# Optimization experiments

Measured on AMD Instinct MI355X. Metric: run time of the kernel, lower is better.

Reference implementation:

```python
import jax, jax.numpy as jnp
import numpy as np

VOCAB = 1024
ENC_D = 256
PRED_D = 256
JOINT_D = ENC_D + PRED_D


def setup_inputs() -> dict:
    key = jax.random.key(0)
    k1, k2, k3, k4, k5, k6 = jax.random.split(key, 6)
    B, T, U = 8, 256, 64
    encoder_outputs = jax.random.normal(k1, (B, T, ENC_D), dtype=jnp.float32)
    decoder_outputs = jax.random.normal(k2, (B, U, PRED_D), dtype=jnp.float32)
    s1 = 1.0 / np.sqrt(JOINT_D)
    W1 = jax.random.uniform(k3, (JOINT_D, JOINT_D), dtype=jnp.float32, minval=-s1, maxval=s1)
    b1 = jax.random.uniform(k4, (JOINT_D,), dtype=jnp.float32, minval=-s1, maxval=s1)
    W2 = jax.random.uniform(k5, (VOCAB, JOINT_D), dtype=jnp.float32, minval=-s1, maxval=s1)
    b2 = jax.random.uniform(k6, (VOCAB,), dtype=jnp.float32, minval=-s1, maxval=s1)
    return {"encoder_outputs": encoder_outputs, "decoder_outputs": decoder_outputs,
            "W1": W1, "b1": b1, "W2": W2, "b2": b2}


def reference(encoder_outputs, decoder_outputs, W1, b1, W2, b2):
    # Decompose the first linear over the concat: split W1 into enc/dec blocks,
    # project each sequence separately, then broadcast-add over (t, u).
    # This is the same math as cat([enc_rep, dec_rep], -1) @ W1.T + b1.
    W1e = W1[:, :ENC_D]   # [J, E]
    W1d = W1[:, ENC_D:]   # [J, P]
    enc_proj = jnp.einsum('bte,je->btj', encoder_outputs, W1e)  # [B,T,J]
    dec_proj = jnp.einsum('bup,jp->buj', decoder_outputs, W1d)  # [B,U,J]
    h = enc_proj[:, :, None, :] + dec_proj[:, None, :, :] + b1  # [B,T,U,J]
    h = jnp.tanh(h)
    logits = jnp.einsum('btuj,vj->btuv', h, W2) + b2             # [B,T,U,V]
    return jax.nn.log_softmax(logits, axis=-1)
```

## Files before the change

### kernel.cpp

```cpp
#include <hip/hip_runtime.h>
#include <hip/hip_bf16.h>
#include <cstdint>
#include <cstddef>

#define NB 8
#define NT 256
#define NU 64
#define DJ 512
#define DV 1024
#define DK 256

typedef __attribute__((ext_vector_type(8))) short short8;
typedef __attribute__((ext_vector_type(4))) float floatx4;

__device__ __forceinline__ unsigned short f2bf(float x) {
    unsigned int u = __float_as_uint(x);
    u += 0x7fffu + ((u >> 16) & 1u);
    return (unsigned short)(u >> 16);
}

__global__ __launch_bounds__(256) void stage1_gemm(
    const float* __restrict__ enc, const float* __restrict__ dec,
    const float* __restrict__ W1, const float* __restrict__ b1,
    float* __restrict__ enc_proj, float* __restrict__ dec_proj)
{
    __shared__ float As[64][17];
    __shared__ float Bs[16][65];

    const int n0 = blockIdx.x * 64;
    const int m0 = blockIdx.y * 64;
    const bool is_enc = (m0 < NB * NT);
    const float* A = is_enc ? enc : dec;
    const int arow0 = is_enc ? m0 : (m0 - NB * NT);
    const int koff  = is_enc ? 0 : DK;
    float* C = is_enc ? enc_proj : dec_proj;

    const int tid = threadIdx.x;
    const int kk = tid & 15;
    const int grp = tid >> 4;
    const int tx = tid & 15;
    const int ty = tid >> 4;

    float acc[4][4] = {};

    for (int k0 = 0; k0 < DK; k0 += 16) {
        #pragma unroll
        for (int g = 0; g < 4; g++) {
            As[grp + g * 16][kk] = A[(size_t)(arow0 + grp + g * 16) * DK + k0 + kk];
            Bs[kk][grp + g * 16] = W1[(size_t)(n0 + grp + g * 16) * DJ + koff + k0 + kk];
        }
        __syncthreads();
        #pragma unroll
        for (int k = 0; k < 16; k++) {
            float av[4], bv[4];
            #pragma unroll
            for (int i = 0; i < 4; i++) av[i] = As[ty * 4 + i][k];
            #pragma unroll
            for (int j = 0; j < 4; j++) bv[j] = Bs[k][tx * 4 + j];
            #pragma unroll
            for (int i = 0; i < 4; i++)
                #pragma unroll
                for (int j = 0; j < 4; j++)
                    acc[i][j] = fmaf(av[i], bv[j], acc[i][j]);
        }
        __syncthreads();
    }

    float4 bias = make_float4(0.f, 0.f, 0.f, 0.f);
    if (is_enc) bias = *(const float4*)&b1[n0 + tx * 4];
    #pragma unroll
    for (int i = 0; i < 4; i++) {
        const int row = arow0 + ty * 4 + i;
        float4 v;
        v.x = acc[i][0] + bias.x;
        v.y = acc[i][1] + bias.y;
        v.z = acc[i][2] + bias.z;
        v.w = acc[i][3] + bias.w;
        *(float4*)&C[(size_t)row * DJ + n0 + tx * 4] = v;
    }
}

__global__ __launch_bounds__(256) void convert_w2(
    const float* __restrict__ W2, unsigned short* __restrict__ W2b)
{
    const int i = (blockIdx.x * 256 + threadIdx.x) * 4;
    float4 v = *(const float4*)(W2 + i);
    ushort4 o;
    o.x = f2bf(v.x); o.y = f2bf(v.y); o.z = f2bf(v.z); o.w = f2bf(v.w);
    *(ushort4*)(W2b + i) = o;
}

__global__ __launch_bounds__(512, 2) void joint_kernel(
    const float* __restrict__ enc_proj, const float* __restrict__ dec_proj,
    const unsigned short* __restrict__ W2b, const float* __restrict__ b2,
    float* __restrict__ out)
{
    __shared__ __align__(16) unsigned char smem[65536];
    unsigned short* ha = (unsigned short*)smem;

    const int bt = blockIdx.x;
    const int b = bt >> 8;
    const int tid = threadIdx.x;

    {
        const int j0 = (tid & 127) * 4;
        const int ug = tid >> 7;
        const float4 e = *(const float4*)(enc_proj + (size_t)bt * DJ + j0);
        const float* dp = dec_proj + (size_t)(b * NU + ug * 16) * DJ + j0;
        const int chunk = j0 >> 3;
        const int wi = j0 & 7;
        #pragma unroll 4
        for (int i = 0; i < 16; i++) {
            const int u = ug * 16 + i;
            float4 d = *(const float4*)(dp + (size_t)i * DJ);
            float x0 = e.x + d.x, x1 = e.y + d.y, x2 = e.z + d.z, x3 = e.w + d.w;
            ushort4 o;
            o.x = f2bf(1.f - 2.f / (__expf(2.f * x0) + 1.f));
            o.y = f2bf(1.f - 2.f / (__expf(2.f * x1) + 1.f));
            o.z = f2bf(1.f - 2.f / (__expf(2.f * x2) + 1.f));
            o.w = f2bf(1.f - 2.f / (__expf(2.f * x3) + 1.f));
            *(ushort4*)(ha + (size_t)u * DJ + (((chunk ^ (u & 7)) << 3) + wi)) = o;
        }
    }
    __syncthreads();

    const int w = tid >> 6;
    const int lane = tid & 63;
    const int q = lane >> 4;
    const int nn = lane & 15;
    const int wbase = w * 128;

    floatx4 acc[4][8];
    #pragma unroll
    for (int rt = 0; rt < 4; rt++)
        #pragma unroll
        for (int ct = 0; ct < 8; ct++)
            acc[rt][ct] = (floatx4){0.f, 0.f, 0.f, 0.f};

    const unsigned short* pB0 = W2b + (size_t)(wbase + nn * 4) * DJ + q * 8;
    const unsigned short* pB1 = pB0 + (size_t)64 * DJ;

    short8 bv0[8], bv1[8];
    short8 av[4];

    #pragma unroll
    for (int c4 = 0; c4 < 4; c4++) {
        bv0[c4]     = *(const short8*)(pB0 + (size_t)c4 * DJ);
        bv0[4 + c4] = *(const short8*)(pB1 + (size_t)c4 * DJ);
    }

    for (int ks = 0; ks < 16; ks += 2) {
        #pragma unroll
        for (int c4 = 0; c4 < 4; c4++) {
            bv1[c4]     = *(const short8*)(pB0 + (size_t)c4 * DJ + (ks + 1) * 32);
            bv1[4 + c4] = *(const short8*)(pB1 + (size_t)c4 * DJ + (ks + 1) * 32);
        }
        #pragma unroll
        for (int rt = 0; rt < 4; rt++) {
            const int u = rt * 16 + nn;
            const int c = ((ks * 4 + q) ^ (u & 7)) << 3;
            av[rt] = *(const short8*)(ha + (size_t)u * DJ + c);
        }
        #pragma unroll
        for (int ct = 0; ct < 8; ct++)
            #pragma unroll
            for (int rt = 0; rt < 4; rt++)
                acc[rt][ct] = __builtin_amdgcn_mfma_f32_16x16x32_bf16(
                    av[rt], bv0[ct], acc[rt][ct], 0, 0, 0);

        if (ks + 2 < 16) {
            #pragma unroll
            for (int c4 = 0; c4 < 4; c4++) {
                bv0[c4]     = *(const short8*)(pB0 + (size_t)c4 * DJ + (ks + 2) * 32);
                bv0[4 + c4] = *(const short8*)(pB1 + (size_t)c4 * DJ + (ks + 2) * 32);
            }
        }
        #pragma unroll
        for (int rt = 0; rt < 4; rt++) {
            const int u = rt * 16 + nn;
            const int c = (((ks + 1) * 4 + q) ^ (u & 7)) << 3;
            av[rt] = *(const short8*)(ha + (size_t)u * DJ + c);
        }
        #pragma unroll
        for (int ct = 0; ct < 8; ct++)
            #pragma unroll
            for (int rt = 0; rt < 4; rt++)
                acc[rt][ct] = __builtin_amdgcn_mfma_f32_16x16x32_bf16(
                    av[rt], bv1[ct], acc[rt][ct], 0, 0, 0);
    }

    __syncthreads();

    float* wred     = (float*)smem;
    float* rowoff_s = (float*)(smem + 2048);

    float b2a[8];
    *(float4*)&b2a[0] = *(const float4*)(b2 + wbase + nn * 4);
    *(float4*)&b2a[4] = *(const float4*)(b2 + wbase + 64 + nn * 4);
    #pragma unroll
    for (int rt = 0; rt < 4; rt++)
        #pragma unroll
        for (int ct = 0; ct < 8; ct++)
            #pragma unroll
            for (int r = 0; r < 4; r++)
                acc[rt][ct][r] += b2a[ct];

    #pragma unroll
    for (int rt = 0; rt < 4; rt++) {
        #pragma unroll
        for (int r = 0; r < 4; r++) {
            float s = 0.f;
            #pragma unroll
            for (int ct = 0; ct < 8; ct++) s += __expf(acc[rt][ct][r]);
            #pragma unroll
            for (int mk = 1; mk <= 8; mk <<= 1) s += __shfl_xor(s, mk, 64);
            if (nn == 0) wred[(rt * 16 + q * 4 + r) * 8 + w] = s;
        }
    }
    __syncthreads();
    if (tid < 64) {
        float4 s0 = *(const float4*)&wred[tid * 8];
        float4 s1 = *(const float4*)&wred[tid * 8 + 4];
        float s = ((s0.x + s0.y) + (s0.z + s0.w)) + ((s1.x + s1.y) + (s1.z + s1.w));
        rowoff_s[tid] = __logf(s);
    }
    __syncthreads();

    float* outb = out + (size_t)bt * NU * DV;
    #pragma unroll
    for (int rt = 0; rt < 4; rt++) {
        #pragma unroll
        for (int r = 0; r < 4; r++) {
            const int u = rt * 16 + q * 4 + r;
            const float off = rowoff_s[u];
            floatx4 v0, v1;
            v0[0] = acc[rt][0][r] - off; v0[1] = acc[rt][1][r] - off;
            v0[2] = acc[rt][2][r] - off; v0[3] = acc[rt][3][r] - off;
            v1[0] = acc[rt][4][r] - off; v1[1] = acc[rt][5][r] - off;
            v1[2] = acc[rt][6][r] - off; v1[3] = acc[rt][7][r] - off;
            __builtin_nontemporal_store(v0, (floatx4*)(outb + (size_t)u * DV + wbase + nn * 4));
            __builtin_nontemporal_store(v1, (floatx4*)(outb + (size_t)u * DV + wbase + 64 + nn * 4));
        }
    }
}

extern "C" void kernel_launch(void* const* d_in, const int* in_sizes, int n_in,
                              void* d_out, int out_size, void* d_ws, size_t ws_size,
                              hipStream_t stream) {
    const float* enc = (const float*)d_in[0];
    const float* dec = (const float*)d_in[1];
    const float* W1  = (const float*)d_in[2];
    const float* b1  = (const float*)d_in[3];
    const float* W2  = (const float*)d_in[4];
    const float* b2  = (const float*)d_in[5];
    float* out = (float*)d_out;

    float* enc_proj = (float*)d_ws;
    float* dec_proj = enc_proj + (size_t)(NB * NT) * DJ;
    unsigned short* W2b = (unsigned short*)(dec_proj + (size_t)DJ * DJ);

    dim3 g1(8, 40);
    stage1_gemm<<<g1, 256, 0, stream>>>(enc, dec, W1, b1, enc_proj, dec_proj);
    convert_w2<<<512, 256, 0, stream>>>(W2, W2b);
    joint_kernel<<<NB * NT, 512, 0, stream>>>(enc_proj, dec_proj, W2b, b2, out);
}
```

Before: 836.4 us.

## Process four timesteps per block with double-buffered tanh prefetch overlapping MFMA

Each joint-kernel block now iterates over four (b,t) rows and keeps two LDS buffers for the tanh hidden tile. While MFMAs consume the current tile, each thread computes and stores the next row's tanh activations into the other buffer. This is meant to hide the tanh/exp prologue and reduce per-block startup. The LDS footprint more than doubles to ~130KB, which limits residency to one block per CU, and the grid shrinks fourfold, reducing parallelism and latency hiding for the output stores.

```diff
diff --git a/kernel.cpp b/kernel.cpp
--- a/kernel.cpp
+++ b/kernel.cpp
@@ -10,6 +10,8 @@
 #define DV 1024
 #define DK 256
 
+#define TPB 4
+
 typedef __attribute__((ext_vector_type(8))) short short8;
 typedef __attribute__((ext_vector_type(4))) float floatx4;
 
@@ -17,6 +19,16 @@
     unsigned int u = __float_as_uint(x);
     u += 0x7fffu + ((u >> 16) & 1u);
     return (unsigned short)(u >> 16);
+}
+
+__device__ __forceinline__ ushort4 tanh4_bf(float4 e, float4 d) {
+    float x0 = e.x + d.x, x1 = e.y + d.y, x2 = e.z + d.z, x3 = e.w + d.w;
+    ushort4 o;
+    o.x = f2bf(1.f - 2.f / (__expf(2.f * x0) + 1.f));
+    o.y = f2bf(1.f - 2.f / (__expf(2.f * x1) + 1.f));
+    o.z = f2bf(1.f - 2.f / (__expf(2.f * x2) + 1.f));
+    o.w = f2bf(1.f - 2.f / (__expf(2.f * x3) + 1.f));
+    return o;
 }
 
 __global__ __launch_bounds__(256) void stage1_gemm(
@@ -95,151 +107,176 @@
     const unsigned short* __restrict__ W2b, const float* __restrict__ b2,
     float* __restrict__ out)
 {
-    __shared__ __align__(16) unsigned char smem[65536];
+    __shared__ __align__(16) unsigned char smem[133376];
     unsigned short* ha = (unsigned short*)smem;
-
-    const int bt = blockIdx.x;
-    const int b = bt >> 8;
+    float* wred     = (float*)(smem + 131072);
+    float* rowoff_s = (float*)(smem + 133120);
+
+    const int bt0 = blockIdx.x * TPB;
     const int tid = threadIdx.x;
 
-    {
-        const int j0 = (tid & 127) * 4;
-        const int ug = tid >> 7;
-        const float4 e = *(const float4*)(enc_proj + (size_t)bt * DJ + j0);
-        const float* dp = dec_proj + (size_t)(b * NU + ug * 16) * DJ + j0;
-        const int chunk = j0 >> 3;
-        const int wi = j0 & 7;
-        #pragma unroll 4
-        for (int i = 0; i < 16; i++) {
-            const int u = ug * 16 + i;
-            float4 d = *(const float4*)(dp + (size_t)i * DJ);
-            float x0 = e.x + d.x, x1 = e.y + d.y, x2 = e.z + d.z, x3 = e.w + d.w;
-            ushort4 o;
-            o.x = f2bf(1.f - 2.f / (__expf(2.f * x0) + 1.f));
-            o.y = f2bf(1.f - 2.f / (__expf(2.f * x1) + 1.f));
-            o.z = f2bf(1.f - 2.f / (__expf(2.f * x2) + 1.f));
-            o.w = f2bf(1.f - 2.f / (__expf(2.f * x3) + 1.f));
-            *(ushort4*)(ha + (size_t)u * DJ + (((chunk ^ (u & 7)) << 3) + wi)) = o;
-        }
-    }
-    __syncthreads();
+    const int j0 = (tid & 127) * 4;
+    const int ug = tid >> 7;
+    const int chunk = j0 >> 3;
+    const int wi = j0 & 7;
 
     const int w = tid >> 6;
     const int lane = tid & 63;
     const int q = lane >> 4;
     const int nn = lane & 15;
     const int wbase = w * 128;
-
-    floatx4 acc[4][8];
-    #pragma unroll
-    for (int rt = 0; rt < 4; rt++)
-        #pragma unroll
-        for (int ct = 0; ct < 8; ct++)
-            acc[rt][ct] = (floatx4){0.f, 0.f, 0.f, 0.f};
-
     const unsigned short* pB0 = W2b + (size_t)(wbase + nn * 4) * DJ + q * 8;
     const unsigned short* pB1 = pB0 + (size_t)64 * DJ;
 
-    short8 bv0[8], bv1[8];
-    short8 av[4];
-
-    #pragma unroll
-    for (int c4 = 0; c4 < 4; c4++) {
-        bv0[c4]     = *(const short8*)(pB0 + (size_t)c4 * DJ);
-        bv0[4 + c4] = *(const short8*)(pB1 + (size_t)c4 * DJ);
-    }
-
-    for (int ks = 0; ks < 16; ks += 2) {
-        #pragma unroll
-        for (int c4 = 0; c4 < 4; c4++) {
-            bv1[c4]     = *(const short8*)(pB0 + (size_t)c4 * DJ + (ks + 1) * 32);
-            bv1[4 + c4] = *(const short8*)(pB1 + (size_t)c4 * DJ + (ks + 1) * 32);
-        }
-        #pragma unroll
-        for (int rt = 0; rt < 4; rt++) {
-            const int u = rt * 16 + nn;
-            const int c = ((ks * 4 + q) ^ (u & 7)) << 3;
-            av[rt] = *(const short8*)(ha + (size_t)u * DJ + c);
-        }
-        #pragma unroll
-        for (int ct = 0; ct < 8; ct++)
-            #pragma unroll
-            for (int rt = 0; rt < 4; rt++)
-                acc[rt][ct] = __builtin_amdgcn_mfma_f32_16x16x32_bf16(
-                    av[rt], bv0[ct], acc[rt][ct], 0, 0, 0);
-
-        if (ks + 2 < 16) {
-            #pragma unroll
-            for (int c4 = 0; c4 < 4; c4++) {
-                bv0[c4]     = *(const short8*)(pB0 + (size_t)c4 * DJ + (ks + 2) * 32);
-                bv0[4 + c4] = *(const short8*)(pB1 + (size_t)c4 * DJ + (ks + 2) * 32);
-            }
-        }
-        #pragma unroll
-        for (int rt = 0; rt < 4; rt++) {
-            const int u = rt * 16 + nn;
-            const int c = (((ks + 1) * 4 + q) ^ (u & 7)) << 3;
-            av[rt] = *(const short8*)(ha + (size_t)u * DJ + c);
-        }
-        #pragma unroll
-        for (int ct = 0; ct < 8; ct++)
-            #pragma unroll
-            for (int rt = 0; rt < 4; rt++)
-                acc[rt][ct] = __builtin_amdgcn_mfma_f32_16x16x32_bf16(
-                    av[rt], bv1[ct], acc[rt][ct], 0, 0, 0);
-    }
-
-    __syncthreads();
-
-    float* wred     = (float*)smem;
-    float* rowoff_s = (float*)(smem + 2048);
-
-    float b2a[8];
-    *(float4*)&b2a[0] = *(const float4*)(b2 + wbase + nn * 4);
-    *(float4*)&b2a[4] = *(const float4*)(b2 + wbase + 64 + nn * 4);
-    #pragma unroll
-    for (int rt = 0; rt < 4; rt++)
-        #pragma unroll
-        for (int ct = 0; ct < 8; ct++)
-            #pragma unroll
-            for (int r = 0; r < 4; r++)
-                acc[rt][ct][r] += b2a[ct];
-
-    #pragma unroll
-    for (int rt = 0; rt < 4; rt++) {
-        #pragma unroll
-        for (int r = 0; r < 4; r++) {
-            float s = 0.f;
-            #pragma unroll
-            for (int ct = 0; ct < 8; ct++) s += __expf(acc[rt][ct][r]);
-            #pragma unroll
-            for (int mk = 1; mk <= 8; mk <<= 1) s += __shfl_xor(s, mk, 64);
-            if (nn == 0) wred[(rt * 16 + q * 4 + r) * 8 + w] = s;
+    {
+        const int bt = bt0;
+        const int b = bt >> 8;
+        const float4 e = *(const float4*)(enc_proj + (size_t)bt * DJ + j0);
+        const float* dpp = dec_proj + (size_t)(b * NU + ug * 16) * DJ + j0;
+        #pragma unroll 4
+        for (int i2 = 0; i2 < 16; i2++) {
+            const int u = ug * 16 + i2;
+            float4 d = *(const float4*)(dpp + (size_t)i2 * DJ);
+            *(ushort4*)(ha + (size_t)u * DJ + (((chunk ^ (u & 7)) << 3) + wi)) =
+                tanh4_bf(e, d);
         }
     }
     __syncthreads();
-    if (tid < 64) {
-        float4 s0 = *(const float4*)&wred[tid * 8];
-        float4 s1 = *(const float4*)&wred[tid * 8 + 4];
-        float s = ((s0.x + s0.y) + (s0.z + s0.w)) + ((s1.x + s1.y) + (s1.z + s1.w));
-        rowoff_s[tid] = __logf(s);
-    }
-    __syncthreads();
-
-    float* outb = out + (size_t)bt * NU * DV;
-    #pragma unroll
-    for (int rt = 0; rt < 4; rt++) {
-        #pragma unroll
-        for (int r = 0; r < 4; r++) {
-            const int u = rt * 16 + q * 4 + r;
-            const float off = rowoff_s[u];
-            floatx4 v0, v1;
-            v0[0] = acc[rt][0][r] - off; v0[1] = acc[rt][1][r] - off;
-            v0[2] = acc[rt][2][r] - off; v0[3] = acc[rt][3][r] - off;
-            v1[0] = acc[rt][4][r] - off; v1[1] = acc[rt][5][r] - off;
-            v1[2] = acc[rt][6][r] - off; v1[3] = acc[rt][7][r] - off;
-            __builtin_nontemporal_store(v0, (floatx4*)(outb + (size_t)u * DV + wbase + nn * 4));
-            __builtin_nontemporal_store(v1, (floatx4*)(outb + (size_t)u * DV + wbase + 64 + nn * 4));
+
+    for (int t = 0; t < TPB; t++) {
+        const int bt = bt0 + t;
+        const int cur = t & 1;
+        unsigned short* hac = ha + cur * 32768;
+        unsigned short* han = ha + (cur ^ 1) * 32768;
+        const bool hasNext = (t + 1 < TPB);
+
+        float4 e_n = make_float4(0.f, 0.f, 0.f, 0.f);
+        const float* dpn = nullptr;
+        float4 dcur = make_float4(0.f, 0.f, 0.f, 0.f);
+        float4 dnxt;
+        if (hasNext) {
+            const int btn = bt + 1;
+            const int bn = btn >> 8;
+            e_n = *(const float4*)(enc_proj + (size_t)btn * DJ + j0);
+            dpn = dec_proj + (size_t)(bn * NU + ug * 16) * DJ + j0;
+            dcur = *(const float4*)(dpn);
+        }
+
+        floatx4 acc[4][8];
+        #pragma unroll
+        for (int rt = 0; rt < 4; rt++)
+            #pragma unroll
+            for (int ct = 0; ct < 8; ct++)
+                acc[rt][ct] = (floatx4){0.f, 0.f, 0.f, 0.f};
+
+        short8 bv0[8], bv1[8];
+        short8 av[4];
+
+        #pragma unroll
+        for (int c4 = 0; c4 < 4; c4++) {
+            bv0[c4]     = *(const short8*)(pB0 + (size_t)c4 * DJ);
+            bv0[4 + c4] = *(const short8*)(pB1 + (size_t)c4 * DJ);
+        }
+
+        for (int ks = 0; ks < 16; ks += 2) {
+            #pragma unroll
+            for (int c4 = 0; c4 < 4; c4++) {
+                bv1[c4]     = *(const short8*)(pB0 + (size_t)c4 * DJ + (ks + 1) * 32);
+                bv1[4 + c4] = *(const short8*)(pB1 + (size_t)c4 * DJ + (ks + 1) * 32);
+            }
+            if (hasNext) {
+                dnxt = *(const float4*)(dpn + (size_t)(ks + 1) * DJ);
+                const int u = ug * 16 + ks;
+                *(ushort4*)(han + (size_t)u * DJ + (((chunk ^ (u & 7)) << 3) + wi)) =
+                    tanh4_bf(e_n, dcur);
+            }
+            #pragma unroll
+            for (int rt = 0; rt < 4; rt++) {
+                const int u2 = rt * 16 + nn;
+                const int c = ((ks * 4 + q) ^ (u2 & 7)) << 3;
+                av[rt] = *(const short8*)(hac + (size_t)u2 * DJ + c);
+            }
+            #pragma unroll
+            for (int ct = 0; ct < 8; ct++)
+                #pragma unroll
+                for (int rt = 0; rt < 4; rt++)
+                    acc[rt][ct] = __builtin_amdgcn_mfma_f32_16x16x32_bf16(
+                        av[rt], bv0[ct], acc[rt][ct], 0, 0, 0);
+
+            if (ks + 2 < 16) {
+                #pragma unroll
+                for (int c4 = 0; c4 < 4; c4++) {
+                    bv0[c4]     = *(const short8*)(pB0 + (size_t)c4 * DJ + (ks + 2) * 32);
+                    bv0[4 + c4] = *(const short8*)(pB1 + (size_t)c4 * DJ + (ks + 2) * 32);
+                }
+            }
+            if (hasNext) {
+                if (ks + 2 < 16) dcur = *(const float4*)(dpn + (size_t)(ks + 2) * DJ);
+                const int u = ug * 16 + ks + 1;
+                *(ushort4*)(han + (size_t)u * DJ + (((chunk ^ (u & 7)) << 3) + wi)) =
+                    tanh4_bf(e_n, dnxt);
+            }
+            #pragma unroll
+            for (int rt = 0; rt < 4; rt++) {
+                const int u2 = rt * 16 + nn;
+                const int c = (((ks + 1) * 4 + q) ^ (u2 & 7)) << 3;
+                av[rt] = *(const short8*)(hac + (size_t)u2 * DJ + c);
+            }
+            #pragma unroll
+            for (int ct = 0; ct < 8; ct++)
+                #pragma unroll
+                for (int rt = 0; rt < 4; rt++)
+                    acc[rt][ct] = __builtin_amdgcn_mfma_f32_16x16x32_bf16(
+                        av[rt], bv1[ct], acc[rt][ct], 0, 0, 0);
+        }
+
+        float b2a[8];
+        *(float4*)&b2a[0] = *(const float4*)(b2 + wbase + nn * 4);
+        *(float4*)&b2a[4] = *(const float4*)(b2 + wbase + 64 + nn * 4);
+        #pragma unroll
+        for (int rt = 0; rt < 4; rt++)
+            #pragma unroll
+            for (int ct = 0; ct < 8; ct++)
+                #pragma unroll
+                for (int r = 0; r < 4; r++)
+                    acc[rt][ct][r] += b2a[ct];
+
+        #pragma unroll
+        for (int rt = 0; rt < 4; rt++) {
+            #pragma unroll
+            for (int r = 0; r < 4; r++) {
+                float s = 0.f;
+                #pragma unroll
+                for (int ct = 0; ct < 8; ct++) s += __expf(acc[rt][ct][r]);
+                #pragma unroll
+                for (int mk = 1; mk <= 8; mk <<= 1) s += __shfl_xor(s, mk, 64);
+                if (nn == 0) wred[(rt * 16 + q * 4 + r) * 8 + w] = s;
+            }
+        }
+        __syncthreads();
+        if (tid < 64) {
+            float4 s0 = *(const float4*)&wred[tid * 8];
+            float4 s1 = *(const float4*)&wred[tid * 8 + 4];
+            float s = ((s0.x + s0.y) + (s0.z + s0.w)) + ((s1.x + s1.y) + (s1.z + s1.w));
+            rowoff_s[tid] = __logf(s);
+        }
+        __syncthreads();
+
+        float* outb = out + (size_t)bt * NU * DV;
+        #pragma unroll
+        for (int rt = 0; rt < 4; rt++) {
+            #pragma unroll
+            for (int r = 0; r < 4; r++) {
+                const int u = rt * 16 + q * 4 + r;
+                const float off = rowoff_s[u];
+                floatx4 v0, v1;
+                v0[0] = acc[rt][0][r] - off; v0[1] = acc[rt][1][r] - off;
+                v0[2] = acc[rt][2][r] - off; v0[3] = acc[rt][3][r] - off;
+                v1[0] = acc[rt][4][r] - off; v1[1] = acc[rt][5][r] - off;
+                v1[2] = acc[rt][6][r] - off; v1[3] = acc[rt][7][r] - off;
+                __builtin_nontemporal_store(v0, (floatx4*)(outb + (size_t)u * DV + wbase + nn * 4));
+                __builtin_nontemporal_store(v1, (floatx4*)(outb + (size_t)u * DV + wbase + 64 + nn * 4));
+            }
         }
     }
 }
@@ -262,5 +299,5 @@
     dim3 g1(8, 40);
     stage1_gemm<<<g1, 256, 0, stream>>>(enc, dec, W1, b1, enc_proj, dec_proj);
     convert_w2<<<512, 256, 0, stream>>>(W2, W2b);
-    joint_kernel<<<NB * NT, 512, 0, stream>>>(enc_proj, dec_proj, W2b, b2, out);
-}
+    joint_kernel<<<(NB * NT) / TPB, 512, 0, stream>>>(enc_proj, dec_proj, W2b, b2, out);
+}
```

New measurement: 843.5 us. Within noise of the previous version (+0.9%).

## Stage W2 tiles through LDS with async global_load_lds double buffering

Applied to the files above, without the earlier changes.

In the joint kernel, the W2 B-operand is no longer loaded straight from global memory into registers. It is now streamed into per-wave LDS buffers with global_load_lds and read back from LDS before each MFMA block. Two buffers split the columns into a low half and a high half, and explicit vmcnt waits plus sched barriers overlap the next load with the current MFMAs. This reduces register use for B fragments from sixteen to four short8 vectors. In exchange, shared memory per block doubles to 128KB, which likely caps occupancy at one 512-thread block per CU and shortens how far ahead B is prefetched.

```diff
diff --git a/kernel.cpp b/kernel.cpp
--- a/kernel.cpp
+++ b/kernel.cpp
@@ -17,6 +17,12 @@
     unsigned int u = __float_as_uint(x);
     u += 0x7fffu + ((u >> 16) & 1u);
     return (unsigned short)(u >> 16);
+}
+
+__device__ __forceinline__ void gll16(const void* g, void* l) {
+    __builtin_amdgcn_global_load_lds(
+        (const __attribute__((address_space(1))) unsigned int*)g,
+        (__attribute__((address_space(3))) unsigned int*)l, 16, 0, 0);
 }
 
 __global__ __launch_bounds__(256) void stage1_gemm(
@@ -95,8 +101,10 @@
     const unsigned short* __restrict__ W2b, const float* __restrict__ b2,
     float* __restrict__ out)
 {
-    __shared__ __align__(16) unsigned char smem[65536];
+    __shared__ __align__(16) unsigned char smem[131072];
     unsigned short* ha = (unsigned short*)smem;
+    unsigned short* Bb0 = (unsigned short*)(smem + 65536);
+    unsigned short* Bb1 = (unsigned short*)(smem + 98304);
 
     const int bt = blockIdx.x;
     const int b = bt >> 8;
@@ -130,6 +138,13 @@
     const int nn = lane & 15;
     const int wbase = w * 128;
 
+    const unsigned short* gpL = W2b + (size_t)(wbase + nn * 4) * DJ + q * 8;
+    const unsigned short* gpH = gpL + (size_t)64 * DJ;
+
+    unsigned short* ldsL = Bb0 + w * 2048;
+    unsigned short* ldsH = Bb1 + w * 2048;
+    const int lrd = lane * 8;
+
     floatx4 acc[4][8];
     #pragma unroll
     for (int rt = 0; rt < 4; rt++)
@@ -137,56 +152,55 @@
         for (int ct = 0; ct < 8; ct++)
             acc[rt][ct] = (floatx4){0.f, 0.f, 0.f, 0.f};
 
-    const unsigned short* pB0 = W2b + (size_t)(wbase + nn * 4) * DJ + q * 8;
-    const unsigned short* pB1 = pB0 + (size_t)64 * DJ;
-
-    short8 bv0[8], bv1[8];
     short8 av[4];
-
-    #pragma unroll
-    for (int c4 = 0; c4 < 4; c4++) {
-        bv0[c4]     = *(const short8*)(pB0 + (size_t)c4 * DJ);
-        bv0[4 + c4] = *(const short8*)(pB1 + (size_t)c4 * DJ);
-    }
-
-    for (int ks = 0; ks < 16; ks += 2) {
-        #pragma unroll
-        for (int c4 = 0; c4 < 4; c4++) {
-            bv1[c4]     = *(const short8*)(pB0 + (size_t)c4 * DJ + (ks + 1) * 32);
-            bv1[4 + c4] = *(const short8*)(pB1 + (size_t)c4 * DJ + (ks + 1) * 32);
-        }
+    short8 bv[4];
+
+    #pragma unroll
+    for (int c4 = 0; c4 < 4; c4++)
+        gll16(gpL + (size_t)c4 * DJ, ldsL + c4 * 512);
+
+    for (int ks = 0; ks < 16; ks++) {
+        #pragma unroll
+        for (int c4 = 0; c4 < 4; c4++)
+            gll16(gpH + (size_t)c4 * DJ + ks * 32, ldsH + c4 * 512);
+
         #pragma unroll
         for (int rt = 0; rt < 4; rt++) {
-            const int u = rt * 16 + nn;
-            const int c = ((ks * 4 + q) ^ (u & 7)) << 3;
-            av[rt] = *(const short8*)(ha + (size_t)u * DJ + c);
-        }
-        #pragma unroll
-        for (int ct = 0; ct < 8; ct++)
+            const int u2 = rt * 16 + nn;
+            const int c = ((ks * 4 + q) ^ (u2 & 7)) << 3;
+            av[rt] = *(const short8*)(ha + (size_t)u2 * DJ + c);
+        }
+
+        asm volatile("s_waitcnt vmcnt(4)" ::: "memory");
+        __builtin_amdgcn_sched_barrier(0);
+        #pragma unroll
+        for (int c4 = 0; c4 < 4; c4++)
+            bv[c4] = *(const short8*)(ldsL + c4 * 512 + lrd);
+        #pragma unroll
+        for (int c4 = 0; c4 < 4; c4++)
             #pragma unroll
             for (int rt = 0; rt < 4; rt++)
-                acc[rt][ct] = __builtin_amdgcn_mfma_f32_16x16x32_bf16(
-                    av[rt], bv0[ct], acc[rt][ct], 0, 0, 0);
-
-        if (ks + 2 < 16) {
-            #pragma unroll
-            for (int c4 = 0; c4 < 4; c4++) {
-                bv0[c4]     = *(const short8*)(pB0 + (size_t)c4 * DJ + (ks + 2) * 32);
-                bv0[4 + c4] = *(const short8*)(pB1 + (size_t)c4 * DJ + (ks + 2) * 32);
-            }
-        }
-        #pragma unroll
-        for (int rt = 0; rt < 4; rt++) {
-            const int u = rt * 16 + nn;
-            const int c = (((ks + 1) * 4 + q) ^ (u & 7)) << 3;
-            av[rt] = *(const short8*)(ha + (size_t)u * DJ + c);
-        }
-        #pragma unroll
-        for (int ct = 0; ct < 8; ct++)
+                acc[rt][c4] = __builtin_amdgcn_mfma_f32_16x16x32_bf16(
+                    av[rt], bv[c4], acc[rt][c4], 0, 0, 0);
+
+        if (ks + 1 < 16) {
+            #pragma unroll
+            for (int c4 = 0; c4 < 4; c4++)
+                gll16(gpL + (size_t)c4 * DJ + (ks + 1) * 32, ldsL + c4 * 512);
+            asm volatile("s_waitcnt vmcnt(4)" ::: "memory");
+        } else {
+            asm volatile("s_waitcnt vmcnt(0)" ::: "memory");
+        }
+        __builtin_amdgcn_sched_barrier(0);
+        #pragma unroll
+        for (int c4 = 0; c4 < 4; c4++)
+            bv[c4] = *(const short8*)(ldsH + c4 * 512 + lrd);
+        #pragma unroll
+        for (int c4 = 0; c4 < 4; c4++)
             #pragma unroll
             for (int rt = 0; rt < 4; rt++)
-                acc[rt][ct] = __builtin_amdgcn_mfma_f32_16x16x32_bf16(
-                    av[rt], bv1[ct], acc[rt][ct], 0, 0, 0);
+                acc[rt][4 + c4] = __builtin_amdgcn_mfma_f32_16x16x32_bf16(
+                    av[rt], bv[c4], acc[rt][4 + c4], 0, 0, 0);
     }
 
     __syncthreads();
```

Measured after the change: 828.4 us. No clear change (-1.0%).
